# Kernel tuning notes

Measured on AMD Instinct MI355X. Metric: run time of the kernel, lower is better.

Reference implementation:

```python
import jax, jax.numpy as jnp
import numpy as np

N_NODES = 100000
N_EDGES = 1200000
D_IN = 64
D_HID = 64
D_OUT = 64


def setup_inputs() -> dict:
    key = jax.random.key(0)
    k1, k2, k3, k4, k5, k6 = jax.random.split(key, 6)
    x = jax.random.normal(k1, (N_NODES, D_IN), dtype=jnp.float32)
    edge_index = jax.random.randint(k2, (2, N_EDGES), 0, N_NODES, dtype=jnp.int32)
    s1 = 1.0 / np.sqrt(2 * D_IN)
    s2 = 1.0 / np.sqrt(2 * D_HID)
    W1 = jax.random.uniform(k3, (2 * D_IN, D_HID), jnp.float32, -s1, s1)
    b1 = jax.random.uniform(k4, (D_HID,), jnp.float32, -s1, s1)
    W2 = jax.random.uniform(k5, (2 * D_HID, D_OUT), jnp.float32, -s2, s2)
    b2 = jax.random.uniform(k6, (D_OUT,), jnp.float32, -s2, s2)
    return {"x": x, "edge_index": edge_index, "W1": W1, "b1": b1, "W2": W2, "b2": b2}


def _sage_conv(x, row, col, W, b):
    n = x.shape[0]
    # gather neighbor features and scatter-sum to destinations
    neighbor_sum = jax.ops.segment_sum(x[col], row, num_segments=n)  # [N, d]
    deg = jax.ops.segment_sum(jnp.ones(row.shape[0], x.dtype), row, num_segments=n)
    deg = jnp.maximum(deg, 1.0)
    neighbor_agg = neighbor_sum / deg[:, None]
    out = jnp.concatenate([x, neighbor_agg], axis=-1)  # [N, 2d]
    return out @ W + b


def reference(x, edge_index, W1, b1, W2, b2):
    row, col = edge_index[0], edge_index[1]
    h = jax.nn.relu(_sage_conv(x, row, col, W1, b1))
    # dropout is identity at inference (training=False)
    return _sage_conv(h, row, col, W2, b2)
```

## Files before the change

kernel.cpp:

```cpp
#include <hip/hip_runtime.h>

#define N_NODES 100000
#define N_EDGES 1200000
#define D 64

#define BSHIFT 8
#define NB ((N_NODES + 255) >> BSHIFT)
#define EPB 2048
#define P1_BLOCKS ((N_EDGES + EPB - 1) / EPB)
#define P2_CAP 4096

#define XSPLIT_BLOCKS (N_NODES * D / 8 / 256)
#define PREP_BLOCKS (XSPLIT_BLOCKS + 64)
#define PC_BLOCKS (PREP_BLOCKS + P1_BLOCKS)

typedef short bf16x8 __attribute__((ext_vector_type(8)));
typedef float f32x4 __attribute__((ext_vector_type(4)));
typedef unsigned short u16x4 __attribute__((ext_vector_type(4)));
typedef unsigned short u16x8 __attribute__((ext_vector_type(8)));

__device__ __forceinline__ short f2bf(float x) {
  unsigned u = __float_as_uint(x);
  unsigned r = (u + 0x7FFFu + ((u >> 16) & 1u)) >> 16;
  return (short)r;
}
__device__ __forceinline__ float bf2f(short b) {
  return __uint_as_float(((unsigned)(unsigned short)b) << 16);
}

__device__ __forceinline__ void w_swz(const float* __restrict__ W,
                                      short* __restrict__ wh,
                                      short* __restrict__ wl, int blk) {
  int i = blk * 256 + threadIdx.x;
  int j = i & 7;
  int l = (i >> 3) & 63;
  int s = (i >> 9) & 3;
  int t = i >> 11;
  int k = s * 32 + ((l >> 4) * 8) + j;
  int n = t * 16 + (l & 15);
  float v = W[k * 64 + n];
  short hb = f2bf(v);
  wh[i] = hb;
  wl[i] = f2bf(v - bf2f(hb));
}

__global__ __launch_bounds__(256) void prep_count(
    const float* __restrict__ x, unsigned short* __restrict__ xh,
    const float* __restrict__ W1, short* __restrict__ w1h, short* __restrict__ w1l,
    const float* __restrict__ W2, short* __restrict__ w2h, short* __restrict__ w2l,
    const int* __restrict__ row, int* __restrict__ bucketCount) {
  const int bid = blockIdx.x;
  const int t = threadIdx.x;
  if (bid < XSPLIT_BLOCKS) {
    int i = bid * 256 + t;
    const float4 a0 = *(const float4*)(x + (size_t)i * 8);
    const float4 a1 = *(const float4*)(x + (size_t)i * 8 + 4);
    const float f[8] = {a0.x, a0.y, a0.z, a0.w, a1.x, a1.y, a1.z, a1.w};
    u16x8 vh;
#pragma unroll
    for (int j = 0; j < 8; ++j) vh[j] = (unsigned short)f2bf(f[j]);
    *(u16x8*)(xh + (size_t)i * 8) = vh;
    return;
  }
  if (bid < XSPLIT_BLOCKS + 32) { w_swz(W1, w1h, w1l, bid - XSPLIT_BLOCKS); return; }
  if (bid < PREP_BLOCKS)        { w_swz(W2, w2h, w2l, bid - XSPLIT_BLOCKS - 32); return; }
  __shared__ int h[NB];
  for (int i = t; i < NB; i += 256) h[i] = 0;
  __syncthreads();
  const int base = (bid - PREP_BLOCKS) * EPB;
#pragma unroll
  for (int i = 0; i < EPB / 256; ++i) {
    int e = base + i * 256 + t;
    if (e < N_EDGES) atomicAdd(&h[row[e] >> BSHIFT], 1);
  }
  __syncthreads();
  for (int i = t; i < NB; i += 256)
    if (h[i]) atomicAdd(&bucketCount[i], h[i]);
}

__global__ __launch_bounds__(512) void p1_scan(const int* __restrict__ bucketCount,
                                               int* __restrict__ bucketStart,
                                               int* __restrict__ cursor) {
  __shared__ int lds[512];
  const int t = threadIdx.x;
  int v = (t < NB) ? bucketCount[t] : 0;
  lds[t] = v;
  __syncthreads();
  for (int off = 1; off < 512; off <<= 1) {
    int add = (t >= off) ? lds[t - off] : 0;
    __syncthreads();
    lds[t] += add;
    __syncthreads();
  }
  if (t < NB) {
    int start = lds[t] - v;
    bucketStart[t] = start;
    cursor[t] = start;
  }
  if (t == NB - 1) bucketStart[NB] = lds[t];
}

__global__ __launch_bounds__(512) void p1_scatter(
    const int* __restrict__ row, const int* __restrict__ col,
    int* __restrict__ cursor, unsigned long long* __restrict__ pairBuf) {
  __shared__ int h[NB];
  __shared__ int hexcl[NB];
  __shared__ int gbase[NB];
  __shared__ int scan_lds[512];
  __shared__ unsigned long long staged[EPB];
  const int t = threadIdx.x;
  for (int i = t; i < NB; i += 512) h[i] = 0;
  __syncthreads();
  const int base = blockIdx.x * EPB;
  const int cnt = min(EPB, N_EDGES - base);

  int myrank[EPB / 512];
  int mybkt[EPB / 512];
  unsigned long long mypair[EPB / 512];
#pragma unroll
  for (int i = 0; i < EPB / 512; ++i) {
    int e = base + i * 512 + t;
    if (e < N_EDGES) {
      unsigned r = (unsigned)row[e];
      unsigned c = (unsigned)col[e];
      int b = (int)(r >> BSHIFT);
      mybkt[i] = b;
      mypair[i] = ((unsigned long long)r << 32) | c;
      myrank[i] = atomicAdd(&h[b], 1);
    } else {
      mybkt[i] = -1;
    }
  }
  __syncthreads();
  int v = (t < NB) ? h[t] : 0;
  scan_lds[t] = v;
  __syncthreads();
  for (int off = 1; off < 512; off <<= 1) {
    int add = (t >= off) ? scan_lds[t - off] : 0;
    __syncthreads();
    scan_lds[t] += add;
    __syncthreads();
  }
  if (t < NB) {
    hexcl[t] = scan_lds[t] - v;
    gbase[t] = (h[t] > 0) ? atomicAdd(&cursor[t], h[t]) : 0;
  }
  __syncthreads();
#pragma unroll
  for (int i = 0; i < EPB / 512; ++i)
    if (mybkt[i] >= 0) staged[hexcl[mybkt[i]] + myrank[i]] = mypair[i];
  __syncthreads();
  for (int i = t; i < cnt; i += 512) {
    unsigned long long p = staged[i];
    int b = (int)(p >> (32 + BSHIFT));
    pairBuf[gbase[b] + (i - hexcl[b])] = p;
  }
}

__global__ __launch_bounds__(256) void p2_csr(
    const unsigned long long* __restrict__ pairBuf,
    const int* __restrict__ bucketStart,
    int* __restrict__ ends, int* __restrict__ sortedCol) {
  __shared__ int hist[256];
  __shared__ int sc[256];
  __shared__ unsigned short rankLDS[P2_CAP];
  const int t = threadIdx.x;
  const int b = blockIdx.x;
  const int base = bucketStart[b];
  const int cnt = min(bucketStart[b + 1] - base, P2_CAP);
  hist[t] = 0;
  __syncthreads();
  for (int i = t; i < cnt; i += 256) {
    int lr = (int)((pairBuf[base + i] >> 32) & ((1 << BSHIFT) - 1));
    rankLDS[i] = (unsigned short)atomicAdd(&hist[lr], 1);
  }
  __syncthreads();
  int v = hist[t];
  sc[t] = v;
  __syncthreads();
  for (int off = 1; off < 256; off <<= 1) {
    int add = (t >= off) ? sc[t - off] : 0;
    __syncthreads();
    sc[t] += add;
    __syncthreads();
  }
  const int node = (b << BSHIFT) + t;
  if (node < N_NODES) ends[node] = base + sc[t];
  const int excl = sc[t] - v;
  __syncthreads();
  sc[t] = excl;
  __syncthreads();
  for (int i = t; i < cnt; i += 256) {
    unsigned long long p = pairBuf[base + i];
    int lr = (int)((p >> 32) & ((1 << BSHIFT) - 1));
    sortedCol[base + sc[lr] + (int)rankLDS[i]] = (int)(unsigned)p;
  }
}

__global__ __launch_bounds__(256) void sage_fused(
    const unsigned short* __restrict__ xsrc, const int* __restrict__ ends,
    const int* __restrict__ sortedCol,
    const short* __restrict__ wh, const short* __restrict__ wl,
    const float* __restrict__ bias, float* __restrict__ outf,
    unsigned short* __restrict__ outb, int doRelu) {
  __shared__ unsigned short aggS[16][72];
  __shared__ int ends_s[17];
  const int tid = threadIdx.x;
  const int w = tid >> 6;
  const int lane = tid & 63;
  const int g = lane >> 4;
  const int fq = lane & 15;
  const int r0 = blockIdx.x * 16;

  if (tid < 17) {
    int idx = r0 - 1 + tid;
    ends_s[tid] = (idx >= 0) ? ends[idx] : 0;
  }
  __syncthreads();

  for (int i = 0; i < 4; ++i) {
    const int rl = w * 4 + i;
    const int start = ends_s[rl];
    const int end = ends_s[rl + 1];
    const int deg = end - start;
    float4 acc = make_float4(0.f, 0.f, 0.f, 0.f);

    for (int base = start; base < end; base += 64) {
      const int m = min(64, end - base);
      const int cv = (lane < m) ? sortedCol[base + lane] : 0;
      for (int j = 0; j < m; j += 16) {
        const int i0 = j + 0 + g, i1 = j + 4 + g, i2 = j + 8 + g, i3 = j + 12 + g;
        const int c0 = __shfl(cv, i0 < m ? i0 : 0);
        const int c1 = __shfl(cv, i1 < m ? i1 : 0);
        const int c2 = __shfl(cv, i2 < m ? i2 : 0);
        const int c3 = __shfl(cv, i3 < m ? i3 : 0);
        u16x4 v0, v1, v2, v3;
        if (i0 < m) v0 = *(const u16x4*)(xsrc + (size_t)c0 * D + fq * 4);
        if (i1 < m) v1 = *(const u16x4*)(xsrc + (size_t)c1 * D + fq * 4);
        if (i2 < m) v2 = *(const u16x4*)(xsrc + (size_t)c2 * D + fq * 4);
        if (i3 < m) v3 = *(const u16x4*)(xsrc + (size_t)c3 * D + fq * 4);
        if (i0 < m) { acc.x += bf2f(v0[0]); acc.y += bf2f(v0[1]);
                      acc.z += bf2f(v0[2]); acc.w += bf2f(v0[3]); }
        if (i1 < m) { acc.x += bf2f(v1[0]); acc.y += bf2f(v1[1]);
                      acc.z += bf2f(v1[2]); acc.w += bf2f(v1[3]); }
        if (i2 < m) { acc.x += bf2f(v2[0]); acc.y += bf2f(v2[1]);
                      acc.z += bf2f(v2[2]); acc.w += bf2f(v2[3]); }
        if (i3 < m) { acc.x += bf2f(v3[0]); acc.y += bf2f(v3[1]);
                      acc.z += bf2f(v3[2]); acc.w += bf2f(v3[3]); }
      }
    }
    acc.x += __shfl_xor(acc.x, 16); acc.x += __shfl_xor(acc.x, 32);
    acc.y += __shfl_xor(acc.y, 16); acc.y += __shfl_xor(acc.y, 32);
    acc.z += __shfl_xor(acc.z, 16); acc.z += __shfl_xor(acc.z, 32);
    acc.w += __shfl_xor(acc.w, 16); acc.w += __shfl_xor(acc.w, 32);
    if (g == 0) {
      const float s = 1.0f / (float)max(deg, 1);
      u16x4 o;
      o[0] = (unsigned short)f2bf(acc.x * s);
      o[1] = (unsigned short)f2bf(acc.y * s);
      o[2] = (unsigned short)f2bf(acc.z * s);
      o[3] = (unsigned short)f2bf(acc.w * s);
      *(u16x4*)(&aggS[rl][fq * 4]) = o;
    }
  }
  __syncthreads();

  const int m = lane & 15;
  const int q = lane >> 4;
  f32x4 acc;
  {
    const float bv = bias[w * 16 + m];
    acc[0] = bv; acc[1] = bv; acc[2] = bv; acc[3] = bv;
  }
#pragma unroll
  for (int s = 0; s < 4; ++s) {
    const int kb = (s & 1) * 32 + q * 8;
    bf16x8 Ah;
    if (s < 2) {
      Ah = *(const bf16x8*)(xsrc + (size_t)(r0 + m) * D + kb);
    } else {
      Ah = *(const bf16x8*)(&aggS[m][kb]);
    }
    const int bi = ((w * 4 + s) * 64 + lane) * 8;
    const bf16x8 Bh = *(const bf16x8*)(wh + bi);
    const bf16x8 Bl = *(const bf16x8*)(wl + bi);
    acc = __builtin_amdgcn_mfma_f32_16x16x32_bf16(Ah, Bh, acc, 0, 0, 0);
    acc = __builtin_amdgcn_mfma_f32_16x16x32_bf16(Ah, Bl, acc, 0, 0, 0);
  }

#pragma unroll
  for (int rg = 0; rg < 4; ++rg) {
    float v = acc[rg];
    const size_t oi = (size_t)(r0 + q * 4 + rg) * D + w * 16 + m;
    if (doRelu) {
      v = fmaxf(v, 0.0f);
      outb[oi] = (unsigned short)f2bf(v);
    } else {
      outf[oi] = v;
    }
  }
}

extern "C" void kernel_launch(void* const* d_in, const int* in_sizes, int n_in,
                              void* d_out, int out_size, void* d_ws, size_t ws_size,
                              hipStream_t stream) {
  const float* x  = (const float*)d_in[0];
  const int*   ei = (const int*)d_in[1];
  const float* W1 = (const float*)d_in[2];
  const float* b1 = (const float*)d_in[3];
  const float* W2 = (const float*)d_in[4];
  const float* b2 = (const float*)d_in[5];
  float* out = (float*)d_out;

  const int* row = ei;
  const int* col = ei + N_EDGES;

  char* ws = (char*)d_ws;
  int* endsArr = (int*)ws;
  size_t off = ((size_t)N_NODES * sizeof(int) + 4095) & ~(size_t)4095;
  int* sortedCol = (int*)(ws + off);
  off += ((size_t)N_EDGES * sizeof(int) + 4095) & ~(size_t)4095;
  int* bucketCount = (int*)(ws + off);
  int* bucketStart = bucketCount + 512;
  int* cursor = bucketStart + 512;
  off += 8192;
  short* w1h = (short*)(ws + off); off += 8192 * sizeof(short);
  short* w1l = (short*)(ws + off); off += 8192 * sizeof(short);
  short* w2h = (short*)(ws + off); off += 8192 * sizeof(short);
  short* w2l = (short*)(ws + off); off += 8192 * sizeof(short);
  unsigned short* xh = (unsigned short*)(ws + off);
  off += (size_t)N_NODES * D * sizeof(unsigned short);
  unsigned short* hh = (unsigned short*)(ws + off);
  off += (size_t)N_NODES * D * sizeof(unsigned short);
  off = (off + 4095) & ~(size_t)4095;
  unsigned long long* pairBuf = (unsigned long long*)(ws + off);

  hipMemsetAsync(bucketCount, 0, NB * sizeof(int), stream);

  prep_count<<<PC_BLOCKS, 256, 0, stream>>>(x, xh, W1, w1h, w1l, W2, w2h, w2l,
                                            row, bucketCount);

  p1_scan<<<1, 512, 0, stream>>>(bucketCount, bucketStart, cursor);
  p1_scatter<<<P1_BLOCKS, 512, 0, stream>>>(row, col, cursor, pairBuf);
  p2_csr<<<NB, 256, 0, stream>>>(pairBuf, bucketStart, endsArr, sortedCol);

  sage_fused<<<N_NODES / 16, 256, 0, stream>>>(xh, endsArr, sortedCol,
                                               w1h, w1l, b1, out, hh, 1);

  sage_fused<<<N_NODES / 16, 256, 0, stream>>>(hh, endsArr, sortedCol,
                                               w2h, w2l, b2, out, hh, 0);
}
```

Before: 213.9 us.

## Assign one destination row per 16-lane group in gather with 8-way unrolled loads

The aggregation is restructured so each wave handles its 4 rows at once, with one 16-lane group per row, instead of looping over rows and splitting each row's edges across four groups. That removes the per-row shuffle reductions and the serial row loop. Each group walks its edge list 8 at a time and issues 8 independent gathers per step to raise memory-level parallelism. The self-feature MFMA operands and the bias are now loaded before the first barrier so they overlap with it. In exchange, rows with very different degrees leave groups in a wave idle, and tail iterations issue clamped redundant loads.

```diff
diff --git a/kernel.cpp b/kernel.cpp
--- a/kernel.cpp
+++ b/kernel.cpp
@@ -216,71 +216,54 @@
     int idx = r0 - 1 + tid;
     ends_s[tid] = (idx >= 0) ? ends[idx] : 0;
   }
-  __syncthreads();
-
-  for (int i = 0; i < 4; ++i) {
-    const int rl = w * 4 + i;
+  const float bv = bias[w * 16 + fq];
+  const bf16x8 self0 = *(const bf16x8*)(xsrc + (size_t)(r0 + fq) * D + g * 8);
+  const bf16x8 self1 = *(const bf16x8*)(xsrc + (size_t)(r0 + fq) * D + 32 + g * 8);
+  __syncthreads();
+
+  {
+    const int rl = w * 4 + g;
     const int start = ends_s[rl];
     const int end = ends_s[rl + 1];
     const int deg = end - start;
     float4 acc = make_float4(0.f, 0.f, 0.f, 0.f);
-
-    for (int base = start; base < end; base += 64) {
-      const int m = min(64, end - base);
-      const int cv = (lane < m) ? sortedCol[base + lane] : 0;
-      for (int j = 0; j < m; j += 16) {
-        const int i0 = j + 0 + g, i1 = j + 4 + g, i2 = j + 8 + g, i3 = j + 12 + g;
-        const int c0 = __shfl(cv, i0 < m ? i0 : 0);
-        const int c1 = __shfl(cv, i1 < m ? i1 : 0);
-        const int c2 = __shfl(cv, i2 < m ? i2 : 0);
-        const int c3 = __shfl(cv, i3 < m ? i3 : 0);
-        u16x4 v0, v1, v2, v3;
-        if (i0 < m) v0 = *(const u16x4*)(xsrc + (size_t)c0 * D + fq * 4);
-        if (i1 < m) v1 = *(const u16x4*)(xsrc + (size_t)c1 * D + fq * 4);
-        if (i2 < m) v2 = *(const u16x4*)(xsrc + (size_t)c2 * D + fq * 4);
-        if (i3 < m) v3 = *(const u16x4*)(xsrc + (size_t)c3 * D + fq * 4);
-        if (i0 < m) { acc.x += bf2f(v0[0]); acc.y += bf2f(v0[1]);
-                      acc.z += bf2f(v0[2]); acc.w += bf2f(v0[3]); }
-        if (i1 < m) { acc.x += bf2f(v1[0]); acc.y += bf2f(v1[1]);
-                      acc.z += bf2f(v1[2]); acc.w += bf2f(v1[3]); }
-        if (i2 < m) { acc.x += bf2f(v2[0]); acc.y += bf2f(v2[1]);
-                      acc.z += bf2f(v2[2]); acc.w += bf2f(v2[3]); }
-        if (i3 < m) { acc.x += bf2f(v3[0]); acc.y += bf2f(v3[1]);
-                      acc.z += bf2f(v3[2]); acc.w += bf2f(v3[3]); }
+    for (int e = start; e < end; e += 8) {
+      int cc[8];
+      u16x4 vv[8];
+#pragma unroll
+      for (int u = 0; u < 8; ++u)
+        cc[u] = sortedCol[min(e + u, end - 1)];
+#pragma unroll
+      for (int u = 0; u < 8; ++u)
+        vv[u] = *(const u16x4*)(xsrc + (size_t)cc[u] * D + fq * 4);
+#pragma unroll
+      for (int u = 0; u < 8; ++u) {
+        if (e + u < end) {
+          acc.x += bf2f((short)vv[u][0]);
+          acc.y += bf2f((short)vv[u][1]);
+          acc.z += bf2f((short)vv[u][2]);
+          acc.w += bf2f((short)vv[u][3]);
+        }
       }
     }
-    acc.x += __shfl_xor(acc.x, 16); acc.x += __shfl_xor(acc.x, 32);
-    acc.y += __shfl_xor(acc.y, 16); acc.y += __shfl_xor(acc.y, 32);
-    acc.z += __shfl_xor(acc.z, 16); acc.z += __shfl_xor(acc.z, 32);
-    acc.w += __shfl_xor(acc.w, 16); acc.w += __shfl_xor(acc.w, 32);
-    if (g == 0) {
-      const float s = 1.0f / (float)max(deg, 1);
-      u16x4 o;
-      o[0] = (unsigned short)f2bf(acc.x * s);
-      o[1] = (unsigned short)f2bf(acc.y * s);
-      o[2] = (unsigned short)f2bf(acc.z * s);
-      o[3] = (unsigned short)f2bf(acc.w * s);
-      *(u16x4*)(&aggS[rl][fq * 4]) = o;
-    }
-  }
-  __syncthreads();
-
-  const int m = lane & 15;
-  const int q = lane >> 4;
+    const float s = 1.0f / (float)max(deg, 1);
+    u16x4 o;
+    o[0] = (unsigned short)f2bf(acc.x * s);
+    o[1] = (unsigned short)f2bf(acc.y * s);
+    o[2] = (unsigned short)f2bf(acc.z * s);
+    o[3] = (unsigned short)f2bf(acc.w * s);
+    *(u16x4*)(&aggS[rl][fq * 4]) = o;
+  }
+  __syncthreads();
+
   f32x4 acc;
-  {
-    const float bv = bias[w * 16 + m];
-    acc[0] = bv; acc[1] = bv; acc[2] = bv; acc[3] = bv;
-  }
+  acc[0] = bv; acc[1] = bv; acc[2] = bv; acc[3] = bv;
 #pragma unroll
   for (int s = 0; s < 4; ++s) {
-    const int kb = (s & 1) * 32 + q * 8;
     bf16x8 Ah;
-    if (s < 2) {
-      Ah = *(const bf16x8*)(xsrc + (size_t)(r0 + m) * D + kb);
-    } else {
-      Ah = *(const bf16x8*)(&aggS[m][kb]);
-    }
+    if (s == 0)      Ah = self0;
+    else if (s == 1) Ah = self1;
+    else             Ah = *(const bf16x8*)(&aggS[fq][(s & 1) * 32 + g * 8]);
     const int bi = ((w * 4 + s) * 64 + lane) * 8;
     const bf16x8 Bh = *(const bf16x8*)(wh + bi);
     const bf16x8 Bl = *(const bf16x8*)(wl + bi);
@@ -291,7 +274,7 @@
 #pragma unroll
   for (int rg = 0; rg < 4; ++rg) {
     float v = acc[rg];
-    const size_t oi = (size_t)(r0 + q * 4 + rg) * D + w * 16 + m;
+    const size_t oi = (size_t)(r0 + g * 4 + rg) * D + w * 16 + fq;
     if (doRelu) {
       v = fmaxf(v, 0.0f);
       outb[oi] = (unsigned short)f2bf(v);
```

After: 210.4 us. About the same (-1.7%).
